# Optimization experiments

Measured on AMD Instinct MI355X. Metric: run time of the kernel, lower is better.

## Reference

```python
import jax, jax.numpy as jnp
import numpy as np

NUM_HEADS = 32
NUM_KV_HEADS = 8
HEAD_DIM = 128
HIDDEN = 4096
THETA = 10000.0


def apply_rotary_emb(x, theta=THETA):
    # x: (B, S, H, D). Torch code converts to complex with real = first half
    # of last dim, imag = second half (rotate-half convention).
    B, S, H, D = x.shape
    half = D // 2
    freqs = 1.0 / theta ** (jnp.arange(0, D, 2, dtype=jnp.float32) / D)  # (half,)
    t = jnp.arange(S, dtype=jnp.float32)
    ang = jnp.outer(t, freqs)  # (S, half)
    cos = jnp.cos(ang)[None, :, None, :]  # (1,S,1,half)
    sin = jnp.sin(ang)[None, :, None, :]
    x1, x2 = x[..., :half], x[..., half:]
    out = jnp.concatenate([x1 * cos - x2 * sin, x1 * sin + x2 * cos], axis=-1)
    return out.astype(x.dtype)


def setup_inputs() -> dict:
    key = jax.random.key(0)
    k1, k2, k3 = jax.random.split(key, 3)
    B, S = 1, 2048
    qkv_out = (NUM_HEADS + 2 * NUM_KV_HEADS) * HEAD_DIM  # 6144
    hidden_states = jax.random.normal(k1, (B, S, HIDDEN), dtype=jnp.float32)
    w_qkv = jax.random.normal(k2, (qkv_out, HIDDEN), dtype=jnp.float32) * 0.02
    w_o = jax.random.normal(k3, (HIDDEN, NUM_HEADS * HEAD_DIM), dtype=jnp.float32) * 0.02
    return {"hidden_states": hidden_states, "w_qkv": w_qkv, "w_o": w_o}


def reference(hidden_states, w_qkv, w_o):
    B, S, _ = hidden_states.shape
    q_size = NUM_HEADS * HEAD_DIM
    kv_size = NUM_KV_HEADS * HEAD_DIM
    n_rep = NUM_HEADS // NUM_KV_HEADS

    qkv = hidden_states @ w_qkv.T  # (B,S,6144)
    xq = qkv[..., :q_size].reshape(B, S, NUM_HEADS, HEAD_DIM)
    xk = qkv[..., q_size:q_size + kv_size].reshape(B, S, NUM_KV_HEADS, HEAD_DIM)
    xv = qkv[..., q_size + kv_size:].reshape(B, S, NUM_KV_HEADS, HEAD_DIM)

    xq = apply_rotary_emb(xq)
    xk = apply_rotary_emb(xk)

    # repeat_interleave KV heads to match query heads
    xk = jnp.repeat(xk, n_rep, axis=2)
    xv = jnp.repeat(xv, n_rep, axis=2)

    q = xq.transpose(0, 2, 1, 3)  # (B,H,S,D)
    k = xk.transpose(0, 2, 1, 3)
    v = xv.transpose(0, 2, 1, 3)

    scale = 1.0 / np.sqrt(HEAD_DIM).astype(np.float32)
    scores = jnp.einsum('bhqd,bhkd->bhqk', q, k) * scale
    causal = jnp.tril(jnp.ones((S, S), dtype=bool))
    scores = jnp.where(causal[None, None], scores, jnp.float32(-jnp.inf))
    attn = jax.nn.softmax(scores, axis=-1)  # dropout=0 (eval)
    out = jnp.einsum('bhqk,bhkd->bhqd', attn, v)
    out = out.transpose(0, 2, 1, 3).reshape(B, S, NUM_HEADS * HEAD_DIM)
    return out @ w_o.T
```

## Files before the change

### kernel.cpp

```cpp
#include <hip/hip_runtime.h>
#include <cstdint>

#define S_LEN 2048
#define HID   4096
#define NHQ   32
#define NKV   8
#define HD    128
#define QKV_N 6144

typedef float  f32x4 __attribute__((ext_vector_type(4)));
typedef short  s16x8 __attribute__((ext_vector_type(8)));
typedef unsigned short ushort_t;

typedef __attribute__((address_space(3))) void       lds_void;
typedef const __attribute__((address_space(1))) void gbl_void;

__device__ __forceinline__ void gload_lds16(const void* g, void* l) {
  __builtin_amdgcn_global_load_lds((gbl_void*)g, (lds_void*)l, 16, 0, 0);
}

__device__ __forceinline__ short f2bf_bits(float f) {
  union { __bf16 b; short s; } u;
  u.b = (__bf16)f;
  return u.s;
}
__device__ __forceinline__ float bf2f(unsigned short u) {
  union { unsigned int i; float f; } x;
  x.i = ((unsigned int)u) << 16;
  return x.f;
}

__global__ __launch_bounds__(256)
void cvt_f32_bf16(const float* __restrict__ src, ushort_t* __restrict__ dst, int n8) {
  int i = blockIdx.x * 256 + threadIdx.x;
  if (i >= n8) return;
  const f32x4* s = (const f32x4*)src;
  f32x4 a = s[i * 2], b = s[i * 2 + 1];
  s16x8 r;
  r[0] = f2bf_bits(a[0]); r[1] = f2bf_bits(a[1]); r[2] = f2bf_bits(a[2]); r[3] = f2bf_bits(a[3]);
  r[4] = f2bf_bits(b[0]); r[5] = f2bf_bits(b[1]); r[6] = f2bf_bits(b[2]); r[7] = f2bf_bits(b[3]);
  *((s16x8*)dst + i) = r;
}

__device__ __forceinline__ s16x8 frag_b16(const char* tile, int row, int quad) {
  return *(const s16x8*)((const ushort_t*)tile + row * 32 + quad * 8);
}

template <bool OUTF32>
__global__ __launch_bounds__(256)
void gemm_bt_bf16(const ushort_t* __restrict__ Ag, const ushort_t* __restrict__ Bg,
                  void* __restrict__ Cp, int M, int N, int K) {
  __shared__ __align__(16) char As[8192];
  __shared__ __align__(16) char Bs[8192];
  const int t = threadIdx.x;
  const int w = t >> 6, l = t & 63;
  const int n16 = l & 15, quad = l >> 4;
  const int m0 = blockIdx.x * 128, n0 = blockIdx.y * 128;
  const int wm = (w >> 1) * 64, wn = (w & 1) * 64;

  f32x4 acc[4][4] = {};

  for (int k0 = 0; k0 < K; k0 += 32) {
#pragma unroll
    for (int c = 0; c < 2; c++) {
      int idx = (w * 2 + c) * 64 + l;
      int row = idx >> 2, csg = idx & 3;
      gload_lds16(Ag + (size_t)(m0 + row) * K + k0 + csg * 8, As + (w * 2 + c) * 1024);
    }
#pragma unroll
    for (int c = 0; c < 2; c++) {
      int idx = (w * 2 + c) * 64 + l;
      int row = idx >> 2, csg = idx & 3;
      gload_lds16(Bg + (size_t)(n0 + row) * K + k0 + csg * 8, Bs + (w * 2 + c) * 1024);
    }
    __syncthreads();

    s16x8 afr[4], bfr[4];
#pragma unroll
    for (int i = 0; i < 4; i++) afr[i] = frag_b16(As, wm + i * 16 + n16, quad);
#pragma unroll
    for (int j = 0; j < 4; j++) bfr[j] = frag_b16(Bs, wn + j * 16 + n16, quad);
#pragma unroll
    for (int i = 0; i < 4; i++)
#pragma unroll
      for (int j = 0; j < 4; j++)
        acc[i][j] = __builtin_amdgcn_mfma_f32_16x16x32_bf16(afr[i], bfr[j], acc[i][j], 0, 0, 0);
    __syncthreads();
  }

#pragma unroll
  for (int i = 0; i < 4; i++)
#pragma unroll
    for (int j = 0; j < 4; j++)
#pragma unroll
      for (int r = 0; r < 4; r++) {
        int row = m0 + wm + i * 16 + quad * 4 + r;
        int col = n0 + wn + j * 16 + n16;
        float v = acc[i][j][r];
        if constexpr (OUTF32) ((float*)Cp)[(size_t)row * N + col] = v;
        else ((ushort_t*)Cp)[(size_t)row * N + col] = (ushort_t)f2bf_bits(v);
      }
}

__global__ __launch_bounds__(256)
void rope_scatter(const ushort_t* __restrict__ qkv, ushort_t* __restrict__ Q,
                  ushort_t* __restrict__ Kc) {
  const int s = blockIdx.x;
  const float LN1E4_64 = 0.14391156831212787f;
  for (int item = threadIdx.x; item < (NHQ + NKV) * 64; item += 256) {
    int head = item >> 6, i = item & 63;
    float f = expf(-(float)i * LN1E4_64);
    float ang = (float)s * f;
    float sn, cs;
    sincosf(ang, &sn, &cs);
    if (head < NHQ) {
      const ushort_t* src = qkv + (size_t)s * QKV_N + head * HD;
      float x1 = bf2f(src[i]), x2 = bf2f(src[64 + i]);
      const float sc = 0.08838834764831845f;
      ushort_t* dst = Q + ((size_t)head * S_LEN + s) * HD;
      dst[i]      = (ushort_t)f2bf_bits((x1 * cs - x2 * sn) * sc);
      dst[64 + i] = (ushort_t)f2bf_bits((x1 * sn + x2 * cs) * sc);
    } else {
      int kv = head - NHQ;
      const ushort_t* src = qkv + (size_t)s * QKV_N + 4096 + kv * HD;
      float x1 = bf2f(src[i]), x2 = bf2f(src[64 + i]);
      ushort_t* dst = Kc + ((size_t)kv * S_LEN + s) * HD;
      dst[i]      = (ushort_t)f2bf_bits(x1 * cs - x2 * sn);
      dst[64 + i] = (ushort_t)f2bf_bits(x1 * sn + x2 * cs);
    }
  }
}

__global__ __launch_bounds__(256)
void v_transpose(const ushort_t* __restrict__ qkv, ushort_t* __restrict__ Vt) {
  __shared__ __align__(16) ushort_t tile[64][72];
  const int s0 = blockIdx.x * 64;
  const int kv = blockIdx.y >> 1;
  const int d0 = (blockIdx.y & 1) * 64;
  const int t = threadIdx.x;
  {
    int r = t >> 2, c = (t & 3) * 16;
    const ushort_t* src = qkv + (size_t)(s0 + r) * QKV_N + 5120 + kv * HD + d0 + c;
    *(s16x8*)&tile[r][c]     = *(const s16x8*)src;
    *(s16x8*)&tile[r][c + 8] = *(const s16x8*)(src + 8);
  }
  __syncthreads();
  {
    int d = t >> 2, sseg = (t & 3) * 16;
    ushort_t* dst = Vt + ((size_t)kv * HD + d0 + d) * S_LEN + s0 + sseg;
    s16x8 o1, o2;
#pragma unroll
    for (int i = 0; i < 8; i++) { o1[i] = tile[sseg + i][d]; o2[i] = tile[sseg + 8 + i][d]; }
    *(s16x8*)dst = o1;
    *(s16x8*)(dst + 8) = o2;
  }
}

__global__ __launch_bounds__(256)
void attn_kernel(const ushort_t* __restrict__ Q, const ushort_t* __restrict__ Kc,
                 const ushort_t* __restrict__ Vt, ushort_t* __restrict__ Out) {
  __shared__ __align__(16) ushort_t Ks[2][64 * 128];
  __shared__ __align__(16) ushort_t Vs[2][128 * 64];
  __shared__ __align__(16) ushort_t Pl[4][16 * 72];
  const int bx = blockIdx.x;
  const int h = blockIdx.y;
  const int t = threadIdx.x, w = t >> 6, l = t & 63;
  const int n16 = l & 15, quad = l >> 4;
  const int kv = h >> 2;
  const ushort_t* Qh = Q  + (size_t)h  * S_LEN * HD;
  const ushort_t* Kh = Kc + (size_t)kv * S_LEN * HD;
  const ushort_t* Vh = Vt + (size_t)kv * HD * S_LEN;

  const int qtA = bx, qtB = 31 - bx;
  const int q0A = qtA * 64 + w * 16, q0B = qtB * 64 + w * 16;
  const int tripsA = qtA + 1;
  const int TOTAL = 33;

  s16x8 qfA[4], qfB[4];
#pragma unroll
  for (int ks = 0; ks < 4; ks++) {
    qfA[ks] = *(const s16x8*)(Qh + (size_t)(q0A + n16) * HD + ks * 32 + quad * 8);
    qfB[ks] = *(const s16x8*)(Qh + (size_t)(q0B + n16) * HD + ks * 32 + quad * 8);
  }

  s16x8 ones;
  {
    short v = (n16 == 0) ? (short)0x3F80 : (short)0;
#pragma unroll
    for (int j = 0; j < 8; j++) ones[j] = v;
  }

  f32x4 o[9] = {};
  float mrun[4] = {-1e30f, -1e30f, -1e30f, -1e30f};

  ushort_t* P = Pl[w];

  auto stage = [&](int k0, int buf) {
#pragma unroll
    for (int c = 0; c < 4; c++) {
      int idx = (c * 4 + w) * 64 + l;
      int row = idx >> 4, sc = idx & 15;
      int dseg = sc ^ (row & 15);
      gload_lds16(Kh + (size_t)(k0 + row) * HD + dseg * 8,
                  (char*)&Ks[buf][0] + (c * 4 + w) * 1024);
    }
#pragma unroll
    for (int c = 0; c < 4; c++) {
      int idx = (c * 4 + w) * 64 + l;
      int row = idx >> 3, sc = idx & 7;
      int ks2 = sc ^ (row & 7);
      gload_lds16(Vh + (size_t)row * S_LEN + k0 + ks2 * 8,
                  (char*)&Vs[buf][0] + (c * 4 + w) * 1024);
    }
  };

  stage(0, 0);

  for (int i = 0; i < TOTAL; i++) {
    const bool isA = (i < tripsA);
    const int kt = isA ? i : i - tripsA;
    const int q0 = isA ? q0A : q0B;
    const int k0 = kt * 64;
    const int buf = i & 1;

    __syncthreads();

    if (i + 1 < TOTAL) {
      const bool nA = (i + 1 < tripsA);
      const int nkt = nA ? (i + 1) : (i + 1 - tripsA);
      stage(nkt * 64, buf ^ 1);
    }

    const ushort_t* KsB = &Ks[buf][0];
    const ushort_t* VsB = &Vs[buf][0];

    f32x4 sacc[4] = {};
#pragma unroll
    for (int ks = 0; ks < 4; ks++) {
      s16x8 qf = isA ? qfA[ks] : qfB[ks];
#pragma unroll
      for (int nt = 0; nt < 4; nt++) {
        int row = nt * 16 + n16;
        s16x8 kf = *(const s16x8*)(KsB + row * 128 + ((ks * 4 + quad) ^ (row & 15)) * 8);
        sacc[nt] = __builtin_amdgcn_mfma_f32_16x16x32_bf16(qf, kf, sacc[nt], 0, 0, 0);
      }
    }

    if (k0 + 63 > q0) {
#pragma unroll
      for (int nt = 0; nt < 4; nt++)
#pragma unroll
        for (int r = 0; r < 4; r++) {
          int qrow = q0 + quad * 4 + r;
          int key  = k0 + nt * 16 + n16;
          if (key > qrow) sacc[nt][r] = -1e30f;
        }
    }

#pragma unroll
    for (int r = 0; r < 4; r++) {
      float tmx = fmaxf(fmaxf(sacc[0][r], sacc[1][r]), fmaxf(sacc[2][r], sacc[3][r]));
#pragma unroll
      for (int d = 1; d < 16; d <<= 1) tmx = fmaxf(tmx, __shfl_xor(tmx, d));
      float nm = fmaxf(mrun[r], tmx);
      float alpha = __expf(mrun[r] - nm);
      mrun[r] = nm;
#pragma unroll
      for (int nt = 0; nt < 4; nt++) sacc[nt][r] = __expf(sacc[nt][r] - nm);
#pragma unroll
      for (int nt2 = 0; nt2 < 9; nt2++) o[nt2][r] *= alpha;
    }

#pragma unroll
    for (int nt = 0; nt < 4; nt++)
#pragma unroll
      for (int r = 0; r < 4; r++)
        P[(quad * 4 + r) * 72 + nt * 16 + n16] = (ushort_t)f2bf_bits(sacc[nt][r]);
    asm volatile("s_waitcnt lgkmcnt(0)" ::: "memory");
    s16x8 pa[2];
#pragma unroll
    for (int kseg = 0; kseg < 2; kseg++)
      pa[kseg] = *(const s16x8*)(P + n16 * 72 + kseg * 32 + quad * 8);

#pragma unroll
    for (int kseg = 0; kseg < 2; kseg++) {
#pragma unroll
      for (int ntd = 0; ntd < 8; ntd++) {
        int row = ntd * 16 + n16;
        s16x8 vf = *(const s16x8*)(VsB + row * 64 + ((kseg * 4 + quad) ^ (row & 7)) * 8);
        o[ntd] = __builtin_amdgcn_mfma_f32_16x16x32_bf16(pa[kseg], vf, o[ntd], 0, 0, 0);
      }
      o[8] = __builtin_amdgcn_mfma_f32_16x16x32_bf16(pa[kseg], ones, o[8], 0, 0, 0);
    }

    if (i == tripsA - 1) {
#pragma unroll
      for (int r = 0; r < 4; r++) {
        float lsum = __shfl(o[8][r], l & 48);
        float inv = 1.0f / lsum;
        int qrow = q0A + quad * 4 + r;
#pragma unroll
        for (int ntd = 0; ntd < 8; ntd++)
          Out[(size_t)qrow * HID + h * HD + ntd * 16 + n16] = (ushort_t)f2bf_bits(o[ntd][r] * inv);
      }
#pragma unroll
      for (int nt2 = 0; nt2 < 9; nt2++) o[nt2] = (f32x4){0.f, 0.f, 0.f, 0.f};
#pragma unroll
      for (int r = 0; r < 4; r++) mrun[r] = -1e30f;
    }
  }

#pragma unroll
  for (int r = 0; r < 4; r++) {
    float lsum = __shfl(o[8][r], l & 48);
    float inv = 1.0f / lsum;
    int qrow = q0B + quad * 4 + r;
#pragma unroll
    for (int ntd = 0; ntd < 8; ntd++)
      Out[(size_t)qrow * HID + h * HD + ntd * 16 + n16] = (ushort_t)f2bf_bits(o[ntd][r] * inv);
  }
}

extern "C" void kernel_launch(void* const* d_in, const int* in_sizes, int n_in,
                              void* d_out, int out_size, void* d_ws, size_t ws_size,
                              hipStream_t stream) {
  const float* hidden = (const float*)d_in[0];
  const float* w_qkv  = (const float*)d_in[1];
  const float* w_o    = (const float*)d_in[2];
  float* out = (float*)d_out;
  char* ws = (char*)d_ws;

  ushort_t* hidden_bf = (ushort_t*)ws;
  ushort_t* Qb        = (ushort_t*)ws;
  ushort_t* wqkv_bf   = (ushort_t*)(ws + 16777216);
  ushort_t* wo_bf     = (ushort_t*)(ws + 16777216);
  ushort_t* qkv       = (ushort_t*)(ws + 67108864);
  ushort_t* attn_out  = (ushort_t*)(ws + 67108864);
  ushort_t* Kb        = (ushort_t*)(ws + 92274688);
  ushort_t* Vtb       = (ushort_t*)(ws + 96468992);

  cvt_f32_bf16<<<dim3(4096),  256, 0, stream>>>(hidden, hidden_bf, 1048576);
  cvt_f32_bf16<<<dim3(12288), 256, 0, stream>>>(w_qkv,  wqkv_bf,   3145728);
  gemm_bt_bf16<false><<<dim3(16, 48), 256, 0, stream>>>(hidden_bf, wqkv_bf, (void*)qkv, 2048, 6144, 4096);
  rope_scatter<<<dim3(2048), 256, 0, stream>>>(qkv, Qb, Kb);
  v_transpose<<<dim3(32, 16), 256, 0, stream>>>(qkv, Vtb);
  cvt_f32_bf16<<<dim3(8192),  256, 0, stream>>>(w_o, wo_bf, 2097152);
  attn_kernel<<<dim3(16, 32), 256, 0, stream>>>(Qb, Kb, Vtb, attn_out);
  gemm_bt_bf16<true><<<dim3(16, 32), 256, 0, stream>>>(attn_out, wo_bf, (void*)out, 2048, 4096, 4096);
}
```

Measured before the change: 543.6 us.

## Double-buffer GEMM LDS tiles and fuse small prep kernels into fewer launches

The bf16 GEMM now keeps two LDS buffers and issues the global-to-LDS loads for the next K slice before computing on the current one. This is meant to overlap memory latency with MFMA work and cut one barrier per iteration. It also precomputes row pointers outside the loop and doubles the GEMM's LDS use, which may lower occupancy. Separately, the hidden and w_qkv conversions are merged into one kernel, and rope, V transpose and w_o conversion are merged into one block-indexed kernel, which reduces launch count and launch gaps.

```diff
diff --git a/kernel.cpp b/kernel.cpp
--- a/kernel.cpp
+++ b/kernel.cpp
@@ -30,62 +30,78 @@
   return x.f;
 }
 
-__global__ __launch_bounds__(256)
-void cvt_f32_bf16(const float* __restrict__ src, ushort_t* __restrict__ dst, int n8) {
-  int i = blockIdx.x * 256 + threadIdx.x;
-  if (i >= n8) return;
+__device__ __forceinline__ void cvt8(const float* src, ushort_t* dst, int j) {
   const f32x4* s = (const f32x4*)src;
-  f32x4 a = s[i * 2], b = s[i * 2 + 1];
+  f32x4 a = s[j * 2], b = s[j * 2 + 1];
   s16x8 r;
   r[0] = f2bf_bits(a[0]); r[1] = f2bf_bits(a[1]); r[2] = f2bf_bits(a[2]); r[3] = f2bf_bits(a[3]);
   r[4] = f2bf_bits(b[0]); r[5] = f2bf_bits(b[1]); r[6] = f2bf_bits(b[2]); r[7] = f2bf_bits(b[3]);
-  *((s16x8*)dst + i) = r;
-}
-
-__device__ __forceinline__ s16x8 frag_b16(const char* tile, int row, int quad) {
-  return *(const s16x8*)((const ushort_t*)tile + row * 32 + quad * 8);
+  *((s16x8*)dst + j) = r;
+}
+
+__global__ __launch_bounds__(256)
+void cvt_hw(const float* __restrict__ h, const float* __restrict__ wq,
+            ushort_t* __restrict__ hb, ushort_t* __restrict__ wqb) {
+  int i = blockIdx.x * 256 + threadIdx.x;
+  if (i < 1048576) cvt8(h, hb, i);
+  else             cvt8(wq, wqb, i - 1048576);
+}
+
+__device__ __forceinline__ s16x8 frag_b16(const ushort_t* tile, int row, int quad) {
+  return *(const s16x8*)(tile + row * 32 + quad * 8);
 }
 
 template <bool OUTF32>
 __global__ __launch_bounds__(256)
 void gemm_bt_bf16(const ushort_t* __restrict__ Ag, const ushort_t* __restrict__ Bg,
                   void* __restrict__ Cp, int M, int N, int K) {
-  __shared__ __align__(16) char As[8192];
-  __shared__ __align__(16) char Bs[8192];
+  __shared__ __align__(16) ushort_t As[2][128 * 32];
+  __shared__ __align__(16) ushort_t Bs[2][128 * 32];
   const int t = threadIdx.x;
   const int w = t >> 6, l = t & 63;
   const int n16 = l & 15, quad = l >> 4;
   const int m0 = blockIdx.x * 128, n0 = blockIdx.y * 128;
   const int wm = (w >> 1) * 64, wn = (w & 1) * 64;
 
+  const int sIdx0 = (w * 2 + 0) * 64 + l;
+  const int sIdx1 = (w * 2 + 1) * 64 + l;
+  const int aRow0 = sIdx0 >> 2, aCs0 = (sIdx0 & 3) * 8;
+  const int aRow1 = sIdx1 >> 2, aCs1 = (sIdx1 & 3) * 8;
+  const ushort_t* Arow0 = Ag + (size_t)(m0 + aRow0) * K + aCs0;
+  const ushort_t* Arow1 = Ag + (size_t)(m0 + aRow1) * K + aCs1;
+  const ushort_t* Brow0 = Bg + (size_t)(n0 + aRow0) * K + aCs0;
+  const ushort_t* Brow1 = Bg + (size_t)(n0 + aRow1) * K + aCs1;
+
   f32x4 acc[4][4] = {};
 
-  for (int k0 = 0; k0 < K; k0 += 32) {
-#pragma unroll
-    for (int c = 0; c < 2; c++) {
-      int idx = (w * 2 + c) * 64 + l;
-      int row = idx >> 2, csg = idx & 3;
-      gload_lds16(Ag + (size_t)(m0 + row) * K + k0 + csg * 8, As + (w * 2 + c) * 1024);
-    }
-#pragma unroll
-    for (int c = 0; c < 2; c++) {
-      int idx = (w * 2 + c) * 64 + l;
-      int row = idx >> 2, csg = idx & 3;
-      gload_lds16(Bg + (size_t)(n0 + row) * K + k0 + csg * 8, Bs + (w * 2 + c) * 1024);
-    }
-    __syncthreads();
-
+  auto stage = [&](int k0, int buf) {
+    gload_lds16(Arow0 + k0, (char*)&As[buf][0] + (w * 2 + 0) * 1024);
+    gload_lds16(Arow1 + k0, (char*)&As[buf][0] + (w * 2 + 1) * 1024);
+    gload_lds16(Brow0 + k0, (char*)&Bs[buf][0] + (w * 2 + 0) * 1024);
+    gload_lds16(Brow1 + k0, (char*)&Bs[buf][0] + (w * 2 + 1) * 1024);
+  };
+  auto compute = [&](int buf) {
     s16x8 afr[4], bfr[4];
 #pragma unroll
-    for (int i = 0; i < 4; i++) afr[i] = frag_b16(As, wm + i * 16 + n16, quad);
-#pragma unroll
-    for (int j = 0; j < 4; j++) bfr[j] = frag_b16(Bs, wn + j * 16 + n16, quad);
+    for (int i = 0; i < 4; i++) afr[i] = frag_b16(&As[buf][0], wm + i * 16 + n16, quad);
+#pragma unroll
+    for (int j = 0; j < 4; j++) bfr[j] = frag_b16(&Bs[buf][0], wn + j * 16 + n16, quad);
 #pragma unroll
     for (int i = 0; i < 4; i++)
 #pragma unroll
       for (int j = 0; j < 4; j++)
         acc[i][j] = __builtin_amdgcn_mfma_f32_16x16x32_bf16(afr[i], bfr[j], acc[i][j], 0, 0, 0);
+  };
+
+  const int nIter = K >> 5;
+  stage(0, 0);
+  for (int it = 0; it < nIter; it += 2) {
     __syncthreads();
+    if (it + 1 < nIter) stage((it + 1) << 5, 1);
+    compute(0);
+    __syncthreads();
+    if (it + 2 < nIter) stage((it + 2) << 5, 0);
+    compute(1);
   }
 
 #pragma unroll
@@ -103,56 +119,62 @@
 }
 
 __global__ __launch_bounds__(256)
-void rope_scatter(const ushort_t* __restrict__ qkv, ushort_t* __restrict__ Q,
-                  ushort_t* __restrict__ Kc) {
-  const int s = blockIdx.x;
-  const float LN1E4_64 = 0.14391156831212787f;
-  for (int item = threadIdx.x; item < (NHQ + NKV) * 64; item += 256) {
-    int head = item >> 6, i = item & 63;
-    float f = expf(-(float)i * LN1E4_64);
-    float ang = (float)s * f;
-    float sn, cs;
-    sincosf(ang, &sn, &cs);
-    if (head < NHQ) {
-      const ushort_t* src = qkv + (size_t)s * QKV_N + head * HD;
-      float x1 = bf2f(src[i]), x2 = bf2f(src[64 + i]);
-      const float sc = 0.08838834764831845f;
-      ushort_t* dst = Q + ((size_t)head * S_LEN + s) * HD;
-      dst[i]      = (ushort_t)f2bf_bits((x1 * cs - x2 * sn) * sc);
-      dst[64 + i] = (ushort_t)f2bf_bits((x1 * sn + x2 * cs) * sc);
-    } else {
-      int kv = head - NHQ;
-      const ushort_t* src = qkv + (size_t)s * QKV_N + 4096 + kv * HD;
-      float x1 = bf2f(src[i]), x2 = bf2f(src[64 + i]);
-      ushort_t* dst = Kc + ((size_t)kv * S_LEN + s) * HD;
-      dst[i]      = (ushort_t)f2bf_bits(x1 * cs - x2 * sn);
-      dst[64 + i] = (ushort_t)f2bf_bits(x1 * sn + x2 * cs);
-    }
-  }
-}
-
-__global__ __launch_bounds__(256)
-void v_transpose(const ushort_t* __restrict__ qkv, ushort_t* __restrict__ Vt) {
+void rope_vt_cvtwo(const ushort_t* __restrict__ qkv, ushort_t* __restrict__ Q,
+                   ushort_t* __restrict__ Kc, ushort_t* __restrict__ Vt,
+                   const float* __restrict__ wo, ushort_t* __restrict__ wob) {
   __shared__ __align__(16) ushort_t tile[64][72];
-  const int s0 = blockIdx.x * 64;
-  const int kv = blockIdx.y >> 1;
-  const int d0 = (blockIdx.y & 1) * 64;
+  const int b = blockIdx.x;
   const int t = threadIdx.x;
-  {
-    int r = t >> 2, c = (t & 3) * 16;
-    const ushort_t* src = qkv + (size_t)(s0 + r) * QKV_N + 5120 + kv * HD + d0 + c;
-    *(s16x8*)&tile[r][c]     = *(const s16x8*)src;
-    *(s16x8*)&tile[r][c + 8] = *(const s16x8*)(src + 8);
-  }
-  __syncthreads();
-  {
-    int d = t >> 2, sseg = (t & 3) * 16;
-    ushort_t* dst = Vt + ((size_t)kv * HD + d0 + d) * S_LEN + s0 + sseg;
-    s16x8 o1, o2;
-#pragma unroll
-    for (int i = 0; i < 8; i++) { o1[i] = tile[sseg + i][d]; o2[i] = tile[sseg + 8 + i][d]; }
-    *(s16x8*)dst = o1;
-    *(s16x8*)(dst + 8) = o2;
+  if (b < 2048) {
+    const int s = b;
+    const float LN1E4_64 = 0.14391156831212787f;
+    for (int item = t; item < (NHQ + NKV) * 64; item += 256) {
+      int head = item >> 6, i = item & 63;
+      float f = expf(-(float)i * LN1E4_64);
+      float ang = (float)s * f;
+      float sn, cs;
+      sincosf(ang, &sn, &cs);
+      if (head < NHQ) {
+        const ushort_t* src = qkv + (size_t)s * QKV_N + head * HD;
+        float x1 = bf2f(src[i]), x2 = bf2f(src[64 + i]);
+        const float sc = 0.08838834764831845f;
+        ushort_t* dst = Q + ((size_t)head * S_LEN + s) * HD;
+        dst[i]      = (ushort_t)f2bf_bits((x1 * cs - x2 * sn) * sc);
+        dst[64 + i] = (ushort_t)f2bf_bits((x1 * sn + x2 * cs) * sc);
+      } else {
+        int kv = head - NHQ;
+        const ushort_t* src = qkv + (size_t)s * QKV_N + 4096 + kv * HD;
+        float x1 = bf2f(src[i]), x2 = bf2f(src[64 + i]);
+        ushort_t* dst = Kc + ((size_t)kv * S_LEN + s) * HD;
+        dst[i]      = (ushort_t)f2bf_bits(x1 * cs - x2 * sn);
+        dst[64 + i] = (ushort_t)f2bf_bits(x1 * sn + x2 * cs);
+      }
+    }
+  } else if (b < 2560) {
+    const int bb = b - 2048;
+    const int s0 = (bb & 31) * 64;
+    const int by = bb >> 5;
+    const int kv = by >> 1;
+    const int d0 = (by & 1) * 64;
+    {
+      int r = t >> 2, c = (t & 3) * 16;
+      const ushort_t* src = qkv + (size_t)(s0 + r) * QKV_N + 5120 + kv * HD + d0 + c;
+      *(s16x8*)&tile[r][c]     = *(const s16x8*)src;
+      *(s16x8*)&tile[r][c + 8] = *(const s16x8*)(src + 8);
+    }
+    __syncthreads();
+    {
+      int d = t >> 2, sseg = (t & 3) * 16;
+      ushort_t* dst = Vt + ((size_t)kv * HD + d0 + d) * S_LEN + s0 + sseg;
+      s16x8 o1, o2;
+#pragma unroll
+      for (int i = 0; i < 8; i++) { o1[i] = tile[sseg + i][d]; o2[i] = tile[sseg + 8 + i][d]; }
+      *(s16x8*)dst = o1;
+      *(s16x8*)(dst + 8) = o2;
+    }
+  } else {
+    int j = (b - 2560) * 256 + t;
+    cvt8(wo, wob, j);
   }
 }
 
@@ -339,12 +361,9 @@
   ushort_t* Kb        = (ushort_t*)(ws + 92274688);
   ushort_t* Vtb       = (ushort_t*)(ws + 96468992);
 
-  cvt_f32_bf16<<<dim3(4096),  256, 0, stream>>>(hidden, hidden_bf, 1048576);
-  cvt_f32_bf16<<<dim3(12288), 256, 0, stream>>>(w_qkv,  wqkv_bf,   3145728);
+  cvt_hw<<<dim3(16384), 256, 0, stream>>>(hidden, w_qkv, hidden_bf, wqkv_bf);
   gemm_bt_bf16<false><<<dim3(16, 48), 256, 0, stream>>>(hidden_bf, wqkv_bf, (void*)qkv, 2048, 6144, 4096);
-  rope_scatter<<<dim3(2048), 256, 0, stream>>>(qkv, Qb, Kb);
-  v_transpose<<<dim3(32, 16), 256, 0, stream>>>(qkv, Vtb);
-  cvt_f32_bf16<<<dim3(8192),  256, 0, stream>>>(w_o, wo_bf, 2097152);
+  rope_vt_cvtwo<<<dim3(10752), 256, 0, stream>>>(qkv, Qb, Kb, Vtb, w_o, wo_bf);
   attn_kernel<<<dim3(16, 32), 256, 0, stream>>>(Qb, Kb, Vtb, attn_out);
   gemm_bt_bf16<true><<<dim3(16, 32), 256, 0, stream>>>(attn_out, wo_bf, (void*)out, 2048, 4096, 4096);
 }
```

Result: faster. 511.6 us (-5.9%).
